# Kernel tuning notes

Measured on AMD Instinct MI355X. Metric: run time of the kernel, lower is better.

The kernel has to match this reference:

```python
import jax, jax.numpy as jnp
import numpy as np

BATCH, TIMESTEPS, DIM, OUT = 64, 512, 1024, 1024


def setup_inputs() -> dict:
    key = jax.random.key(0)
    k1, k2, k3, k4, k5, k6 = jax.random.split(key, 6)
    # glorot-normal-ish scales for params
    def glorot(k, shape):
        fan_in, fan_out = shape[0], shape[-1]
        std = (2.0 / (fan_in + fan_out)) ** 0.5
        return jax.random.normal(k, shape, dtype=jnp.float32) * std
    return {
        "inputs": jax.random.normal(k1, (BATCH, TIMESTEPS, DIM), dtype=jnp.float32),
        "prev_state": jax.random.normal(k2, (BATCH, OUT), dtype=jnp.float32),
        "Wa": glorot(k3, (OUT, OUT)),
        "Ua": glorot(k4, (DIM, OUT)),
        "Va": glorot(k5, (OUT, 1)),
        "Ba": glorot(k6, (1, OUT)),
    }


def reference(inputs, prev_state, Wa, Ua, Va, Ba):
    # WaS: [B, 1, OUT] broadcast over timesteps
    WaS = jnp.einsum("bo,op->bp", prev_state, Wa)[:, None, :]
    # UaH: [B, T, OUT]
    UaH = jnp.einsum("btd,do->bto", inputs, Ua)
    scores = jnp.tanh(UaH + WaS + Ba)            # [B, T, OUT]
    scores = jax.nn.relu(scores @ Va)            # [B, T, 1]
    sm = jax.nn.softmax(scores, axis=1)          # softmax over timesteps
    context_vector = jnp.sum(inputs * sm, axis=1)  # [B, DIM]
    return context_vector
```

## Files before the change

kernel.cpp:

```cpp
#include <hip/hip_runtime.h>


#define NBATCH 64
#define NT     512
#define NDIM   1024
#define NOUT   1024

typedef _Float16 h8 __attribute__((ext_vector_type(8)));
typedef _Float16 h4 __attribute__((ext_vector_type(4)));
typedef float f16v __attribute__((ext_vector_type(16)));

__device__ __forceinline__ float tanh_fast(float x) {
    float e = __expf(2.0f * x);
    return 1.0f - 2.0f * __builtin_amdgcn_rcpf(e + 1.0f);
}

__global__ __launch_bounds__(256) void k_pack_ua(const float* __restrict__ Ua,
                                                 _Float16* __restrict__ B16) {
    int t = blockIdx.x * 256 + threadIdx.x;
    int k = t >> 10, n = t & 1023;
    int nt = n >> 5, nn = n & 31;
    int ks = k >> 4, kg = (k >> 3) & 1, j = k & 7;
    int pos = (((nt << 6) + ks) << 9) + (((kg << 5) + nn) << 3) + j;
    B16[pos] = (_Float16)Ua[t];
}

__global__ __launch_bounds__(256) void k_was_part(const float* __restrict__ ps,
                                                  const float* __restrict__ Wa,
                                                  float* __restrict__ part) {
    int oc = blockIdx.x, b = blockIdx.y, tid = threadIdx.x;
    const float4* Wa4 = (const float4*)Wa;
    const float* psb = ps + b * 1024;
    float4 acc = {0.f, 0.f, 0.f, 0.f};
    int o0 = oc * 128;
#pragma unroll 4
    for (int o = o0; o < o0 + 128; ++o) {
        float s = psb[o];
        float4 wv = Wa4[o * 256 + tid];
        acc.x += s * wv.x; acc.y += s * wv.y; acc.z += s * wv.z; acc.w += s * wv.w;
    }
    ((float4*)part)[((oc << 6) + b) * 256 + tid] = acc;
}

__global__ __launch_bounds__(256) void k_was_reduce(const float* __restrict__ part,
                                                    const float* __restrict__ Ba,
                                                    float* __restrict__ wsWaS) {
    int b = blockIdx.x, tid = threadIdx.x;
    const float4* p4 = (const float4*)part;
    float4 acc = ((const float4*)Ba)[tid];
#pragma unroll
    for (int oc = 0; oc < 8; ++oc) {
        float4 v = p4[((oc << 6) + b) * 256 + tid];
        acc.x += v.x; acc.y += v.y; acc.z += v.z; acc.w += v.w;
    }
    ((float4*)wsWaS)[b * 256 + tid] = acc;
}

#define ASH_STRIDE 136
__global__ __launch_bounds__(256, 2) void k_fused_gemm(
    const float* __restrict__ inputs, const _Float16* __restrict__ B16,
    const float* __restrict__ wsWaS, const float* __restrict__ Va,
    float* __restrict__ scores)
{
    __shared__ _Float16 Ash[64 * ASH_STRIDE];
    __shared__ float scoreSh[64];
    const int tid = threadIdx.x;
    const int lane = tid & 63, wv = tid >> 6;
    const int l31 = lane & 31, lhi = lane >> 5;
    const int r0 = blockIdx.x * 64;
    const int b = r0 >> 9;
    const int srow = tid >> 2, sq = tid & 3;
    const float4* inF4 = (const float4*)inputs;

    if (tid < 64) scoreSh[tid] = 0.0f;

    for (int pass = 0; pass < 2; ++pass) {
        const int c0w = pass * 512 + wv * 128;
        const int ntb = c0w >> 5;
        f16v acc[2][4];
#pragma unroll
        for (int rt = 0; rt < 2; ++rt)
#pragma unroll
            for (int ct = 0; ct < 4; ++ct)
#pragma unroll
                for (int e = 0; e < 16; ++e) acc[rt][ct][e] = 0.0f;

        for (int kc = 0; kc < 8; ++kc) {
            const int k0 = kc * 128;
            __syncthreads();
            {
                const float4* src = inF4 + (size_t)(r0 + srow) * 256 + (k0 >> 2) + sq * 8;
                _Float16* dst = &Ash[srow * ASH_STRIDE + sq * 32];
#pragma unroll
                for (int jj = 0; jj < 8; ++jj) {
                    float4 v = src[jj];
                    h4 hv = { (_Float16)v.x, (_Float16)v.y, (_Float16)v.z, (_Float16)v.w };
                    *(h4*)(dst + jj * 4) = hv;
                }
            }
            __syncthreads();
#pragma unroll
            for (int ks8 = 0; ks8 < 8; ++ks8) {
                const int ks = kc * 8 + ks8;
                h8 a0 = *(const h8*)&Ash[l31 * ASH_STRIDE + ks8 * 16 + lhi * 8];
                h8 a1 = *(const h8*)&Ash[(32 + l31) * ASH_STRIDE + ks8 * 16 + lhi * 8];
#pragma unroll
                for (int ct = 0; ct < 4; ++ct) {
                    const h8 bf = *(const h8*)(B16 +
                        ((size_t)(((ntb + ct) << 6) + ks) << 9) + lane * 8);
                    acc[0][ct] = __builtin_amdgcn_mfma_f32_32x32x16_f16(a0, bf, acc[0][ct], 0, 0, 0);
                    acc[1][ct] = __builtin_amdgcn_mfma_f32_32x32x16_f16(a1, bf, acc[1][ct], 0, 0, 0);
                }
            }
        }
        float wsv[4], vav[4];
#pragma unroll
        for (int ct = 0; ct < 4; ++ct) {
            int n = c0w + ct * 32 + l31;
            wsv[ct] = wsWaS[b * 1024 + n];
            vav[ct] = Va[n];
        }
#pragma unroll
        for (int rt = 0; rt < 2; ++rt) {
#pragma unroll
            for (int i = 0; i < 16; ++i) {
                float s = 0.0f;
#pragma unroll
                for (int ct = 0; ct < 4; ++ct)
                    s += tanh_fast(acc[rt][ct][i] + wsv[ct]) * vav[ct];
                s += __shfl_xor(s, 1);
                s += __shfl_xor(s, 2);
                s += __shfl_xor(s, 4);
                s += __shfl_xor(s, 8);
                s += __shfl_xor(s, 16);
                if (l31 == 0) {
                    int row = rt * 32 + (i & 3) + ((i >> 2) << 3) + (lhi << 2);
                    atomicAdd(&scoreSh[row], s);
                }
            }
        }
    }
    __syncthreads();
    if (tid < 64) scores[r0 + tid] = fmaxf(scoreSh[tid], 0.0f);
}

__global__ __launch_bounds__(256) void k_softmax(const float* __restrict__ scores,
                                                 float* __restrict__ sm) {
    int b = blockIdx.x, tid = threadIdx.x;
    __shared__ float red[256];
    const float* sb = scores + b * 512;
    float s0 = sb[tid], s1 = sb[tid + 256];
    red[tid] = fmaxf(s0, s1);
    __syncthreads();
    for (int st = 128; st > 0; st >>= 1) {
        if (tid < st) red[tid] = fmaxf(red[tid], red[tid + st]);
        __syncthreads();
    }
    float m = red[0];
    __syncthreads();
    float e0 = __expf(s0 - m), e1 = __expf(s1 - m);
    red[tid] = e0 + e1;
    __syncthreads();
    for (int st = 128; st > 0; st >>= 1) {
        if (tid < st) red[tid] += red[tid + st];
        __syncthreads();
    }
    float inv = 1.0f / red[0];
    sm[b * 512 + tid] = e0 * inv;
    sm[b * 512 + 256 + tid] = e1 * inv;
}

__global__ __launch_bounds__(256) void k_ctx_part(const float* __restrict__ inputs,
                                                  const float* __restrict__ sm,
                                                  float* __restrict__ part) {
    int ts = blockIdx.x, b = blockIdx.y, tid = threadIdx.x;
    const float4* inF4 = (const float4*)inputs;
    float4 acc = {0.f, 0.f, 0.f, 0.f};
    int t0 = ts * 64;
#pragma unroll 4
    for (int t = t0; t < t0 + 64; ++t) {
        float wgt = sm[b * 512 + t];
        float4 x = inF4[(size_t)(b * 512 + t) * 256 + tid];
        acc.x += wgt * x.x; acc.y += wgt * x.y; acc.z += wgt * x.z; acc.w += wgt * x.w;
    }
    ((float4*)part)[((ts << 6) + b) * 256 + tid] = acc;
}

__global__ __launch_bounds__(256) void k_ctx_reduce(const float* __restrict__ part,
                                                    float* __restrict__ out) {
    int g = blockIdx.x * 256 + threadIdx.x;
    const float4* p4 = (const float4*)part;
    float4 acc = p4[g];
#pragma unroll
    for (int s = 1; s < 8; ++s) {
        float4 v = p4[s * 16384 + g];
        acc.x += v.x; acc.y += v.y; acc.z += v.z; acc.w += v.w;
    }
    ((float4*)out)[g] = acc;
}

extern "C" void kernel_launch(void* const* d_in, const int* in_sizes, int n_in,
                              void* d_out, int out_size, void* d_ws, size_t ws_size,
                              hipStream_t stream) {
    const float* inputs = (const float*)d_in[0];
    const float* prev   = (const float*)d_in[1];
    const float* Wa     = (const float*)d_in[2];
    const float* Ua     = (const float*)d_in[3];
    const float* Va     = (const float*)d_in[4];
    const float* Ba     = (const float*)d_in[5];
    float* out = (float*)d_out;

    char* ws = (char*)d_ws;
    _Float16* B16   = (_Float16*)(ws);
    float* wasPart  = (float*)(ws + (2u << 20));
    float* wsWaS    = (float*)(ws + (4u << 20));
    float* scores   = (float*)(ws + (4u << 20) + (256u << 10));
    float* sm       = (float*)(ws + (4u << 20) + (384u << 10));
    float* ctxPart  = (float*)(ws + (4u << 20) + (512u << 10));

    hipLaunchKernelGGL(k_pack_ua,    dim3(4096),   dim3(256), 0, stream, Ua, B16);
    hipLaunchKernelGGL(k_was_part,   dim3(8, 64),  dim3(256), 0, stream, prev, Wa, wasPart);
    hipLaunchKernelGGL(k_was_reduce, dim3(64),     dim3(256), 0, stream, wasPart, Ba, wsWaS);
    hipLaunchKernelGGL(k_fused_gemm, dim3(512),    dim3(256), 0, stream, inputs, B16, wsWaS, Va, scores);
    hipLaunchKernelGGL(k_softmax,    dim3(64),     dim3(256), 0, stream, scores, sm);
    hipLaunchKernelGGL(k_ctx_part,   dim3(8, 64),  dim3(256), 0, stream, inputs, sm, ctxPart);
    hipLaunchKernelGGL(k_ctx_reduce, dim3(64),     dim3(256), 0, stream, ctxPart, out);
}
```

Before: 346.8 us.

## Double-buffer A tiles in fused GEMM and vectorize Ua packing writes

After: 342.6 us. Within noise of the previous version (-1.2%).

```diff
diff --git a/kernel.cpp b/kernel.cpp
--- a/kernel.cpp
+++ b/kernel.cpp
@@ -18,11 +18,13 @@
 __global__ __launch_bounds__(256) void k_pack_ua(const float* __restrict__ Ua,
                                                  _Float16* __restrict__ B16) {
     int t = blockIdx.x * 256 + threadIdx.x;
-    int k = t >> 10, n = t & 1023;
-    int nt = n >> 5, nn = n & 31;
-    int ks = k >> 4, kg = (k >> 3) & 1, j = k & 7;
-    int pos = (((nt << 6) + ks) << 9) + (((kg << 5) + nn) << 3) + j;
-    B16[pos] = (_Float16)Ua[t];
+    int nn = t & 31, kg = (t >> 5) & 1, ks = (t >> 6) & 63, nt = t >> 12;
+    int n = (nt << 5) + nn;
+    int kbase = (ks << 4) + (kg << 3);
+    h8 v;
+#pragma unroll
+    for (int j = 0; j < 8; ++j) v[j] = (_Float16)Ua[(size_t)(kbase + j) * 1024 + n];
+    *(h8*)(B16 + ((size_t)t << 3)) = v;
 }
 
 __global__ __launch_bounds__(256) void k_was_part(const float* __restrict__ ps,
@@ -62,7 +64,7 @@
     const float* __restrict__ wsWaS, const float* __restrict__ Va,
     float* __restrict__ scores)
 {
-    __shared__ _Float16 Ash[64 * ASH_STRIDE];
+    __shared__ _Float16 Ash[2][64 * ASH_STRIDE];
     __shared__ float scoreSh[64];
     const int tid = threadIdx.x;
     const int lane = tid & 63, wv = tid >> 6;
@@ -70,9 +72,23 @@
     const int r0 = blockIdx.x * 64;
     const int b = r0 >> 9;
     const int srow = tid >> 2, sq = tid & 3;
-    const float4* inF4 = (const float4*)inputs;
+    const float4* srcBase = (const float4*)inputs + (size_t)(r0 + srow) * 256 + sq * 8;
 
     if (tid < 64) scoreSh[tid] = 0.0f;
+
+    float4 vA[8];
+#pragma unroll
+    for (int j = 0; j < 8; ++j) vA[j] = srcBase[j];
+    {
+        _Float16* dst = &Ash[0][srow * ASH_STRIDE + sq * 32];
+#pragma unroll
+        for (int j = 0; j < 8; ++j) {
+            float4 v = vA[j];
+            *(h4*)(dst + j * 4) =
+                (h4){ (_Float16)v.x, (_Float16)v.y, (_Float16)v.z, (_Float16)v.w };
+        }
+    }
+    __syncthreads();
 
     for (int pass = 0; pass < 2; ++pass) {
         const int c0w = pass * 512 + wv * 128;
@@ -86,32 +102,39 @@
                 for (int e = 0; e < 16; ++e) acc[rt][ct][e] = 0.0f;
 
         for (int kc = 0; kc < 8; ++kc) {
-            const int k0 = kc * 128;
-            __syncthreads();
-            {
-                const float4* src = inF4 + (size_t)(r0 + srow) * 256 + (k0 >> 2) + sq * 8;
-                _Float16* dst = &Ash[srow * ASH_STRIDE + sq * 32];
-#pragma unroll
-                for (int jj = 0; jj < 8; ++jj) {
-                    float4 v = src[jj];
-                    h4 hv = { (_Float16)v.x, (_Float16)v.y, (_Float16)v.z, (_Float16)v.w };
-                    *(h4*)(dst + jj * 4) = hv;
-                }
-            }
-            __syncthreads();
+            const int buf = kc & 1;
+            const bool pf = !(pass == 1 && kc == 7);
+            if (pf) {
+                const float4* src = srcBase + (((kc + 1) & 7) << 5);
+#pragma unroll
+                for (int j = 0; j < 8; ++j) vA[j] = src[j];
+            }
 #pragma unroll
             for (int ks8 = 0; ks8 < 8; ++ks8) {
                 const int ks = kc * 8 + ks8;
-                h8 a0 = *(const h8*)&Ash[l31 * ASH_STRIDE + ks8 * 16 + lhi * 8];
-                h8 a1 = *(const h8*)&Ash[(32 + l31) * ASH_STRIDE + ks8 * 16 + lhi * 8];
+                h8 a0 = *(const h8*)&Ash[buf][l31 * ASH_STRIDE + ks8 * 16 + lhi * 8];
+                h8 a1 = *(const h8*)&Ash[buf][(32 + l31) * ASH_STRIDE + ks8 * 16 + lhi * 8];
+                h8 bf[4];
+#pragma unroll
+                for (int ct = 0; ct < 4; ++ct)
+                    bf[ct] = *(const h8*)(B16 +
+                        ((size_t)(((ntb + ct) << 6) + ks) << 9) + lane * 8);
 #pragma unroll
                 for (int ct = 0; ct < 4; ++ct) {
-                    const h8 bf = *(const h8*)(B16 +
-                        ((size_t)(((ntb + ct) << 6) + ks) << 9) + lane * 8);
-                    acc[0][ct] = __builtin_amdgcn_mfma_f32_32x32x16_f16(a0, bf, acc[0][ct], 0, 0, 0);
-                    acc[1][ct] = __builtin_amdgcn_mfma_f32_32x32x16_f16(a1, bf, acc[1][ct], 0, 0, 0);
+                    acc[0][ct] = __builtin_amdgcn_mfma_f32_32x32x16_f16(a0, bf[ct], acc[0][ct], 0, 0, 0);
+                    acc[1][ct] = __builtin_amdgcn_mfma_f32_32x32x16_f16(a1, bf[ct], acc[1][ct], 0, 0, 0);
                 }
             }
+            if (pf) {
+                _Float16* dst = &Ash[buf ^ 1][srow * ASH_STRIDE + sq * 32];
+#pragma unroll
+                for (int j = 0; j < 8; ++j) {
+                    float4 v = vA[j];
+                    *(h4*)(dst + j * 4) =
+                        (h4){ (_Float16)v.x, (_Float16)v.y, (_Float16)v.z, (_Float16)v.w };
+                }
+            }
+            __syncthreads();
         }
         float wsv[4], vav[4];
 #pragma unroll
@@ -177,7 +200,7 @@
     const float4* inF4 = (const float4*)inputs;
     float4 acc = {0.f, 0.f, 0.f, 0.f};
     int t0 = ts * 64;
-#pragma unroll 4
+#pragma unroll 8
     for (int t = t0; t < t0 + 64; ++t) {
         float wgt = sm[b * 512 + t];
         float4 x = inF4[(size_t)(b * 512 + t) * 256 + tid];
@@ -218,7 +241,7 @@
     float* sm       = (float*)(ws + (4u << 20) + (384u << 10));
     float* ctxPart  = (float*)(ws + (4u << 20) + (512u << 10));
 
-    hipLaunchKernelGGL(k_pack_ua,    dim3(4096),   dim3(256), 0, stream, Ua, B16);
+    hipLaunchKernelGGL(k_pack_ua,    dim3(512),    dim3(256), 0, stream, Ua, B16);
     hipLaunchKernelGGL(k_was_part,   dim3(8, 64),  dim3(256), 0, stream, prev, Wa, wasPart);
     hipLaunchKernelGGL(k_was_reduce, dim3(64),     dim3(256), 0, stream, wasPart, Ba, wsWaS);
     hipLaunchKernelGGL(k_fused_gemm, dim3(512),    dim3(256), 0, stream, inputs, B16, wsWaS, Va, scores);
```
